# Performance work log

Measured on AMD Instinct MI355X. Metric: run time of the kernel, lower is better.

Reference implementation:

```python
import jax, jax.numpy as jnp
import numpy as np

B, Q, K, DQ, DK, DV, H = 4, 256, 1024, 512, 512, 512, 128
MASK_VALUE = -1e6  # matches torch sequence_mask fill of -1000000.0


def setup_inputs() -> dict:
    key = jax.random.key(0)
    ks = jax.random.split(key, 7)
    q = jax.random.normal(ks[0], (B, Q, DQ), dtype=jnp.float32)
    k = jax.random.normal(ks[1], (B, K, DK), dtype=jnp.float32)
    v = jax.random.normal(ks[2], (B, K, DV), dtype=jnp.float32)
    valid_lens = jax.random.randint(ks[3], (B,), 1, K + 1).astype(jnp.int64)
    # Linear weights stored torch-style as [out, in]
    w_q = jax.random.normal(ks[4], (H, DQ), dtype=jnp.float32) * 0.05
    w_k = jax.random.normal(ks[5], (H, DK), dtype=jnp.float32) * 0.05
    w_v = jax.random.normal(ks[6], (H,), dtype=jnp.float32) * 0.05
    return {"q": q, "k": k, "v": v, "valid_lens": valid_lens,
            "w_q": w_q, "w_k": w_k, "w_v": w_v}


def reference(q, k, v, valid_lens, w_q, w_k, w_v):
    qh = jnp.einsum("bqd,hd->bqh", q, w_q)              # [B,Q,H]
    kh = jnp.einsum("bkd,hd->bkh", k, w_k)              # [B,K,H]
    feats = jnp.tanh(qh[:, :, None, :] + kh[:, None, :, :])  # [B,Q,K,H]
    scores = jnp.einsum("bqkh,h->bqk", feats, w_v)      # [B,Q,K]
    mask = jnp.arange(K)[None, None, :] < valid_lens[:, None, None]
    scores = jnp.where(mask, scores, MASK_VALUE)
    attn = jax.nn.softmax(scores, axis=-1)              # dropout is identity (p=0)
    return jnp.einsum("bqk,bkv->bqv", attn, v)          # [B,Q,DV]
```

## Files before the change

### kernel.cpp

```cpp
#include <hip/hip_runtime.h>

#define B_ 4
#define Q_ 256
#define K_ 1024
#define D_ 512
#define H_ 128
#define DV_ 512
#define LOG2E 1.4426950408889634f


__global__ __launch_bounds__(256) void proj_part(
    const float* __restrict__ qin, const float* __restrict__ kin,
    const float* __restrict__ wq,  const float* __restrict__ wk,
    const int* __restrict__ valid_lens, float* __restrict__ psum)
{
    __shared__ float Xs[64][68];
    __shared__ float Ws[64][132];

    const int t = threadIdx.x, bid = blockIdx.x;
    const int ds = bid & 7, tile = bid >> 3;
    const int d0 = ds * 64;
    const float* X; const float* W;
    if (tile < 16) { X = qin + (size_t)tile * 64 * D_; W = wq; }
    else {
        int kt = tile - 16, b = kt >> 4, kr = (kt & 15) * 64;
        if (kr >= valid_lens[b]) return;
        X = kin + ((size_t)b * K_ + kr) * D_;
        W = wk;
    }
    const int R0 = tile * 64;

#pragma unroll
    for (int i = 0; i < 4; ++i) {
        int idx = t + i * 256;
        int row = idx >> 4, dq = (idx & 15) * 4;
        float4 xv = *(const float4*)&X[(size_t)row * D_ + d0 + dq];
        Xs[dq+0][row] = xv.x; Xs[dq+1][row] = xv.y;
        Xs[dq+2][row] = xv.z; Xs[dq+3][row] = xv.w;
    }
#pragma unroll
    for (int i = 0; i < 8; ++i) {
        int idx = t + i * 256;
        int h = idx >> 4, dq = (idx & 15) * 4;
        float4 wv = *(const float4*)&W[(size_t)h * D_ + d0 + dq];
        Ws[dq+0][h] = wv.x; Ws[dq+1][h] = wv.y;
        Ws[dq+2][h] = wv.z; Ws[dq+3][h] = wv.w;
    }
    __syncthreads();

    const int wid = t >> 6, lane = t & 63;
    const int r0 = (wid >> 1) * 32 + (lane >> 3) * 4;
    const int h0 = (wid & 1)  * 64 + (lane & 7)  * 8;
    float c[4][8] = {};

#pragma unroll 4
    for (int kk = 0; kk < 64; ++kk) {
        float xr[4], wr[8];
        *(float4*)&xr[0] = *(const float4*)&Xs[kk][r0];
        *(float4*)&wr[0] = *(const float4*)&Ws[kk][h0];
        *(float4*)&wr[4] = *(const float4*)&Ws[kk][h0 + 4];
#pragma unroll
        for (int i = 0; i < 4; ++i)
#pragma unroll
            for (int j = 0; j < 8; ++j) c[i][j] += xr[i] * wr[j];
    }

    float* outp = psum + ((size_t)ds * 5120 + R0) * 128;
#pragma unroll
    for (int i = 0; i < 4; ++i) {
        *(float4*)&outp[(size_t)(r0 + i) * 128 + h0]     = *(const float4*)&c[i][0];
        *(float4*)&outp[(size_t)(r0 + i) * 128 + h0 + 4] = *(const float4*)&c[i][4];
    }
}

__global__ __launch_bounds__(256) void proj_reduce(
    const float* __restrict__ psum, const int* __restrict__ valid_lens,
    float* __restrict__ qh_s, float4* __restrict__ kh4)
{
    int gid = blockIdx.x * 256 + threadIdx.x;
    int row = gid >> 5, c4 = gid & 31;
    int b = 0, kk = 0;
    if (row >= 1024) {
        int r = row - 1024;
        b = r >> 10; kk = r & 1023;
        if (kk >= valid_lens[b]) return;
    }
    float4 s = make_float4(0.f, 0.f, 0.f, 0.f);
#pragma unroll
    for (int ds = 0; ds < 8; ++ds) {
        float4 v = *(const float4*)&psum[((size_t)ds * 5120 + row) * 128 + c4 * 4];
        s.x += v.x; s.y += v.y; s.z += v.z; s.w += v.w;
    }
    const float SC = 2.0f * LOG2E;
    s.x *= SC; s.y *= SC; s.z *= SC; s.w *= SC;
    if (row < 1024) *(float4*)&qh_s[(size_t)row * 128 + c4 * 4] = s;
    else            kh4[((size_t)(b * 32 + c4)) * K_ + kk] = s;
}

__global__ __launch_bounds__(256) void attn_part(
    const float* __restrict__ qh_s, const float4* __restrict__ kh4,
    const float* __restrict__ wvg,  const int* __restrict__ valid_lens,
    const float* __restrict__ vin,
    float* __restrict__ s_part, float4* __restrict__ o_part)
{
    __shared__ float  qv[1024];
    __shared__ float  wvs[128];
    __shared__ float  ptmp[3][8][64];
    __shared__ float  p[8][64];
    __shared__ float4 otmp[8][128];

    const int t   = threadIdx.x;
    const int bid = blockIdx.x;
    const int qt  = bid & 31, kc = (bid >> 5) & 15, b = bid >> 9;
    const int q0  = qt * 8;
    const int vl  = valid_lens[b];
    const int kbase = kc * 64;
    if (kbase >= vl) return;
    const int klen = min(64, vl - kbase);

#pragma unroll
    for (int i = 0; i < 4; ++i)
        qv[t + i * 256] = qh_s[(size_t)(b*Q_ + q0) * H_ + t + i * 256];
    if (t < 128) wvs[t] = wvg[t] * (-2.0f * LOG2E);
    __syncthreads();

    const int k  = t & 63;
    const int hh = t >> 6;
    const bool active = k < klen;

    float acc[8] = {};
    if (active) {
        const float4* khp = kh4 + (size_t)b * 32 * K_ + (kbase + k)
                          + (size_t)(hh * 8) * K_;
        const int hq0 = hh * 8;
        float4 kxn = khp[0];
#pragma unroll
        for (int i = 0; i < 8; ++i) {
            float4 kx = kxn;
            int ni = (i < 7) ? i + 1 : 7;
            kxn = khp[(size_t)ni * K_];
            const int hq = hq0 + i;
            float w4[4], kxa[4];
            *(float4*)&w4[0]  = *(const float4*)&wvs[hq*4];
            *(float4*)&kxa[0] = kx;
#pragma unroll
            for (int qi = 0; qi < 8; ++qi) {
                float q4[4];
                *(float4*)&q4[0] = *(const float4*)&qv[qi*128 + hq*4];
#pragma unroll
                for (int j = 0; j < 4; ++j) {
                    float tt = __builtin_amdgcn_exp2f(q4[j] + kxa[j]);
                    float rr = __builtin_amdgcn_rcpf(tt + 1.0f);
                    acc[qi] = fmaf(w4[j], rr, acc[qi]);
                }
            }
        }
    }
    if (hh != 0) {
#pragma unroll
        for (int qi = 0; qi < 8; ++qi) ptmp[hh-1][qi][k] = acc[qi];
    }
    __syncthreads();

    if (hh == 0) {
        float psum8[8];
#pragma unroll
        for (int qi = 0; qi < 8; ++qi) {
            float a = acc[qi] + ptmp[0][qi][k] + ptmp[1][qi][k] + ptmp[2][qi][k];
            float e = active ? __builtin_amdgcn_exp2f(a) : 0.f;
            p[qi][k] = e;
            psum8[qi] = e;
        }
#pragma unroll
        for (int off = 32; off > 0; off >>= 1)
#pragma unroll
            for (int qi = 0; qi < 8; ++qi) psum8[qi] += __shfl_xor(psum8[qi], off);
        if (t == 0) {
#pragma unroll
            for (int qi = 0; qi < 8; ++qi)
                s_part[(size_t)(b*Q_ + q0 + qi) * 16 + kc] = psum8[qi];
        }
    }
    __syncthreads();

    const int col  = t & 127;
    const int half = t >> 7;
    const int kb2  = half * 32;
    const int ke2  = min(klen, kb2 + 32);
    const float4* vb = (const float4*)vin + (size_t)b * K_ * 128
                     + (size_t)kbase * 128;

    float4 o[8];
#pragma unroll
    for (int qi = 0; qi < 8; ++qi) o[qi] = make_float4(0.f, 0.f, 0.f, 0.f);

    int kk = kb2;
    const int nfull = (ke2 > kb2) ? ((ke2 - kb2) >> 2) : 0;
    if (nfull > 0) {
        float4 n0v = vb[(size_t)(kk+0)*128 + col];
        float4 n1v = vb[(size_t)(kk+1)*128 + col];
        float4 n2v = vb[(size_t)(kk+2)*128 + col];
        float4 n3v = vb[(size_t)(kk+3)*128 + col];
        for (int g = 0; g < nfull; ++g) {
            float4 v0 = n0v, v1 = n1v, v2 = n2v, v3 = n3v;
            int kn = kk + 4;
            if (g + 1 < nfull) {
                n0v = vb[(size_t)(kn+0)*128 + col];
                n1v = vb[(size_t)(kn+1)*128 + col];
                n2v = vb[(size_t)(kn+2)*128 + col];
                n3v = vb[(size_t)(kn+3)*128 + col];
            }
#pragma unroll
            for (int qi = 0; qi < 8; ++qi) {
                float4 pq = *(const float4*)&p[qi][kk];
                o[qi].x += pq.x*v0.x + pq.y*v1.x + pq.z*v2.x + pq.w*v3.x;
                o[qi].y += pq.x*v0.y + pq.y*v1.y + pq.z*v2.y + pq.w*v3.y;
                o[qi].z += pq.x*v0.z + pq.y*v1.z + pq.z*v2.z + pq.w*v3.z;
                o[qi].w += pq.x*v0.w + pq.y*v1.w + pq.z*v2.w + pq.w*v3.w;
            }
            kk = kn;
        }
    }
    for (; kk < ke2; ++kk) {
        float4 v0 = vb[(size_t)kk*128 + col];
#pragma unroll
        for (int qi = 0; qi < 8; ++qi) {
            float pk = p[qi][kk];
            o[qi].x += pk*v0.x; o[qi].y += pk*v0.y;
            o[qi].z += pk*v0.z; o[qi].w += pk*v0.w;
        }
    }

    if (half == 1) {
#pragma unroll
        for (int qi = 0; qi < 8; ++qi) otmp[qi][col] = o[qi];
    }
    __syncthreads();
    if (half == 0) {
#pragma unroll
        for (int qi = 0; qi < 8; ++qi) {
            float4 r = otmp[qi][col];
            o[qi].x += r.x; o[qi].y += r.y; o[qi].z += r.z; o[qi].w += r.w;
            o_part[((size_t)kc * 1024 + (b*Q_ + q0 + qi)) * 128 + col] = o[qi];
        }
    }
}

__global__ __launch_bounds__(256) void finalize_kernel(
    const float4* __restrict__ o_part, const float* __restrict__ s_part,
    const int* __restrict__ valid_lens, float4* __restrict__ out)
{
    int gid = blockIdx.x * 256 + threadIdx.x;
    int row = gid >> 7, col = gid & 127;
    int b = row >> 8;
    int nch = (valid_lens[b] + 63) >> 6;
    float ssum = 0.f;
    float4 o = make_float4(0.f, 0.f, 0.f, 0.f);
    for (int ch = 0; ch < nch; ++ch) {
        ssum += s_part[(size_t)row * 16 + ch];
        float4 r = o_part[((size_t)ch * 1024 + row) * 128 + col];
        o.x += r.x; o.y += r.y; o.z += r.z; o.w += r.w;
    }
    float rs = __builtin_amdgcn_rcpf(ssum);
    out[gid] = make_float4(o.x*rs, o.y*rs, o.z*rs, o.w*rs);
}

extern "C" void kernel_launch(void* const* d_in, const int* in_sizes, int n_in,
                              void* d_out, int out_size, void* d_ws, size_t ws_size,
                              hipStream_t stream)
{
    const float* q  = (const float*)d_in[0];
    const float* k  = (const float*)d_in[1];
    const float* v  = (const float*)d_in[2];
    const int*   vl = (const int*)d_in[3];
    const float* wq = (const float*)d_in[4];
    const float* wk = (const float*)d_in[5];
    const float* wv = (const float*)d_in[6];
    float* out = (float*)d_out;

    float* qh_s  = (float*)d_ws;
    float* kh4   = qh_s  + (size_t)B_*Q_*H_;
    float* s_prt = kh4   + (size_t)B_*H_*K_;
    float* o_prt = s_prt + (size_t)B_*Q_*16;
    float* psum  = o_prt + (size_t)16*B_*Q_*DV_;

    proj_part      <<<dim3(640),  dim3(256), 0, stream>>>(q, k, wq, wk, vl, psum);
    proj_reduce    <<<dim3(640),  dim3(256), 0, stream>>>(psum, vl, qh_s, (float4*)kh4);
    attn_part      <<<dim3(2048), dim3(256), 0, stream>>>(qh_s, (const float4*)kh4, wv, vl, v, s_prt, (float4*)o_prt);
    finalize_kernel<<<dim3(512),  dim3(256), 0, stream>>>((const float4*)o_prt, s_prt, vl, (float4*)out);
}
```

Baseline: 115.3 us.

## Fuse projection reduction via atomics and widen attention key chunks to 128

Removes the proj_reduce kernel and its partial-sum buffer. proj_part now pre-scales the weights and atomically accumulates its split-D partials straight into zeroed qh/kh buffers, with a memset added up front. Separately, attn_part now takes 128-key chunks with two head-halves per thread group instead of 64 keys with four, which halves the block count and the number of finalize partials. The trade-off is many scattered float atomics in a strided kh layout, an extra memset, and possibly lower occupancy from the doubled per-thread head loop.

Measured after the change: 295.6 us. 156% more time.

```diff
diff --git a/kernel.cpp b/kernel.cpp
--- a/kernel.cpp
+++ b/kernel.cpp
@@ -12,7 +12,8 @@
 __global__ __launch_bounds__(256) void proj_part(
     const float* __restrict__ qin, const float* __restrict__ kin,
     const float* __restrict__ wq,  const float* __restrict__ wk,
-    const int* __restrict__ valid_lens, float* __restrict__ psum)
+    const int* __restrict__ valid_lens,
+    float* __restrict__ qh_s, float* __restrict__ khf)
 {
     __shared__ float Xs[64][68];
     __shared__ float Ws[64][132];
@@ -21,14 +22,18 @@
     const int ds = bid & 7, tile = bid >> 3;
     const int d0 = ds * 64;
     const float* X; const float* W;
-    if (tile < 16) { X = qin + (size_t)tile * 64 * D_; W = wq; }
+    int kb = 0, kr0 = 0;
+    bool is_q;
+    if (tile < 16) { X = qin + (size_t)tile * 64 * D_; W = wq; is_q = true; }
     else {
-        int kt = tile - 16, b = kt >> 4, kr = (kt & 15) * 64;
-        if (kr >= valid_lens[b]) return;
-        X = kin + ((size_t)b * K_ + kr) * D_;
+        int kt = tile - 16; kb = kt >> 4; kr0 = (kt & 15) * 64;
+        if (kr0 >= valid_lens[kb]) return;
+        X = kin + ((size_t)kb * K_ + kr0) * D_;
         W = wk;
+        is_q = false;
     }
     const int R0 = tile * 64;
+    const float SC = 2.0f * LOG2E;
 
 #pragma unroll
     for (int i = 0; i < 4; ++i) {
@@ -43,8 +48,8 @@
         int idx = t + i * 256;
         int h = idx >> 4, dq = (idx & 15) * 4;
         float4 wv = *(const float4*)&W[(size_t)h * D_ + d0 + dq];
-        Ws[dq+0][h] = wv.x; Ws[dq+1][h] = wv.y;
-        Ws[dq+2][h] = wv.z; Ws[dq+3][h] = wv.w;
+        Ws[dq+0][h] = wv.x * SC; Ws[dq+1][h] = wv.y * SC;
+        Ws[dq+2][h] = wv.z * SC; Ws[dq+3][h] = wv.w * SC;
     }
     __syncthreads();
 
@@ -65,36 +70,25 @@
             for (int j = 0; j < 8; ++j) c[i][j] += xr[i] * wr[j];
     }
 
-    float* outp = psum + ((size_t)ds * 5120 + R0) * 128;
-#pragma unroll
-    for (int i = 0; i < 4; ++i) {
-        *(float4*)&outp[(size_t)(r0 + i) * 128 + h0]     = *(const float4*)&c[i][0];
-        *(float4*)&outp[(size_t)(r0 + i) * 128 + h0 + 4] = *(const float4*)&c[i][4];
-    }
-}
-
-__global__ __launch_bounds__(256) void proj_reduce(
-    const float* __restrict__ psum, const int* __restrict__ valid_lens,
-    float* __restrict__ qh_s, float4* __restrict__ kh4)
-{
-    int gid = blockIdx.x * 256 + threadIdx.x;
-    int row = gid >> 5, c4 = gid & 31;
-    int b = 0, kk = 0;
-    if (row >= 1024) {
-        int r = row - 1024;
-        b = r >> 10; kk = r & 1023;
-        if (kk >= valid_lens[b]) return;
-    }
-    float4 s = make_float4(0.f, 0.f, 0.f, 0.f);
-#pragma unroll
-    for (int ds = 0; ds < 8; ++ds) {
-        float4 v = *(const float4*)&psum[((size_t)ds * 5120 + row) * 128 + c4 * 4];
-        s.x += v.x; s.y += v.y; s.z += v.z; s.w += v.w;
-    }
-    const float SC = 2.0f * LOG2E;
-    s.x *= SC; s.y *= SC; s.z *= SC; s.w *= SC;
-    if (row < 1024) *(float4*)&qh_s[(size_t)row * 128 + c4 * 4] = s;
-    else            kh4[((size_t)(b * 32 + c4)) * K_ + kk] = s;
+    if (is_q) {
+#pragma unroll
+        for (int i = 0; i < 4; ++i) {
+            float* rp = qh_s + (size_t)(R0 + r0 + i) * 128 + h0;
+#pragma unroll
+            for (int j = 0; j < 8; ++j) atomicAdd(&rp[j], c[i][j]);
+        }
+    } else {
+#pragma unroll
+        for (int i = 0; i < 4; ++i) {
+            int kk = kr0 + r0 + i;
+#pragma unroll
+            for (int j = 0; j < 8; ++j) {
+                int h = h0 + j;
+                size_t idx = (((size_t)kb * 32 + (h >> 2)) * K_ + kk) * 4 + (h & 3);
+                atomicAdd(&khf[idx], c[i][j]);
+            }
+        }
+    }
 }
 
 __global__ __launch_bounds__(256) void attn_part(
@@ -105,18 +99,19 @@
 {
     __shared__ float  qv[1024];
     __shared__ float  wvs[128];
-    __shared__ float  ptmp[3][8][64];
-    __shared__ float  p[8][64];
+    __shared__ float  ptmp[8][128];
+    __shared__ float  p[8][128];
+    __shared__ float  sred[2][8];
     __shared__ float4 otmp[8][128];
 
     const int t   = threadIdx.x;
     const int bid = blockIdx.x;
-    const int qt  = bid & 31, kc = (bid >> 5) & 15, b = bid >> 9;
+    const int qt  = bid & 31, kc = (bid >> 5) & 7, b = bid >> 8;
     const int q0  = qt * 8;
     const int vl  = valid_lens[b];
-    const int kbase = kc * 64;
+    const int kbase = kc * 128;
     if (kbase >= vl) return;
-    const int klen = min(64, vl - kbase);
+    const int klen = min(128, vl - kbase);
 
 #pragma unroll
     for (int i = 0; i < 4; ++i)
@@ -124,22 +119,21 @@
     if (t < 128) wvs[t] = wvg[t] * (-2.0f * LOG2E);
     __syncthreads();
 
-    const int k  = t & 63;
-    const int hh = t >> 6;
+    const int k  = t & 127;
+    const int hh = t >> 7;
     const bool active = k < klen;
 
     float acc[8] = {};
     if (active) {
         const float4* khp = kh4 + (size_t)b * 32 * K_ + (kbase + k)
-                          + (size_t)(hh * 8) * K_;
-        const int hq0 = hh * 8;
+                          + (size_t)(hh * 16) * K_;
         float4 kxn = khp[0];
-#pragma unroll
-        for (int i = 0; i < 8; ++i) {
+#pragma unroll 4
+        for (int i = 0; i < 16; ++i) {
             float4 kx = kxn;
-            int ni = (i < 7) ? i + 1 : 7;
+            int ni = (i < 15) ? i + 1 : 15;
             kxn = khp[(size_t)ni * K_];
-            const int hq = hq0 + i;
+            const int hq = hh * 16 + i;
             float w4[4], kxa[4];
             *(float4*)&w4[0]  = *(const float4*)&wvs[hq*4];
             *(float4*)&kxa[0] = kx;
@@ -156,9 +150,9 @@
             }
         }
     }
-    if (hh != 0) {
-#pragma unroll
-        for (int qi = 0; qi < 8; ++qi) ptmp[hh-1][qi][k] = acc[qi];
+    if (hh == 1) {
+#pragma unroll
+        for (int qi = 0; qi < 8; ++qi) ptmp[qi][k] = acc[qi];
     }
     __syncthreads();
 
@@ -166,7 +160,7 @@
         float psum8[8];
 #pragma unroll
         for (int qi = 0; qi < 8; ++qi) {
-            float a = acc[qi] + ptmp[0][qi][k] + ptmp[1][qi][k] + ptmp[2][qi][k];
+            float a = acc[qi] + ptmp[qi][k];
             float e = active ? __builtin_amdgcn_exp2f(a) : 0.f;
             p[qi][k] = e;
             psum8[qi] = e;
@@ -175,18 +169,23 @@
         for (int off = 32; off > 0; off >>= 1)
 #pragma unroll
             for (int qi = 0; qi < 8; ++qi) psum8[qi] += __shfl_xor(psum8[qi], off);
-        if (t == 0) {
-#pragma unroll
-            for (int qi = 0; qi < 8; ++qi)
-                s_part[(size_t)(b*Q_ + q0 + qi) * 16 + kc] = psum8[qi];
-        }
-    }
-    __syncthreads();
+        if ((t & 63) == 0) {
+#pragma unroll
+            for (int qi = 0; qi < 8; ++qi) sred[t >> 6][qi] = psum8[qi];
+        }
+    }
+    __syncthreads();
+
+    if (t == 0) {
+#pragma unroll
+        for (int qi = 0; qi < 8; ++qi)
+            s_part[(size_t)(b*Q_ + q0 + qi) * 8 + kc] = sred[0][qi] + sred[1][qi];
+    }
 
     const int col  = t & 127;
     const int half = t >> 7;
-    const int kb2  = half * 32;
-    const int ke2  = min(klen, kb2 + 32);
+    const int kb2  = half * 64;
+    const int ke2  = min(klen, kb2 + 64);
     const float4* vb = (const float4*)vin + (size_t)b * K_ * 128
                      + (size_t)kbase * 128;
 
@@ -253,11 +252,11 @@
     int gid = blockIdx.x * 256 + threadIdx.x;
     int row = gid >> 7, col = gid & 127;
     int b = row >> 8;
-    int nch = (valid_lens[b] + 63) >> 6;
+    int nch = (valid_lens[b] + 127) >> 7;
     float ssum = 0.f;
     float4 o = make_float4(0.f, 0.f, 0.f, 0.f);
     for (int ch = 0; ch < nch; ++ch) {
-        ssum += s_part[(size_t)row * 16 + ch];
+        ssum += s_part[(size_t)row * 8 + ch];
         float4 r = o_part[((size_t)ch * 1024 + row) * 128 + col];
         o.x += r.x; o.y += r.y; o.z += r.z; o.w += r.w;
     }
@@ -281,11 +280,11 @@
     float* qh_s  = (float*)d_ws;
     float* kh4   = qh_s  + (size_t)B_*Q_*H_;
     float* s_prt = kh4   + (size_t)B_*H_*K_;
-    float* o_prt = s_prt + (size_t)B_*Q_*16;
-    float* psum  = o_prt + (size_t)16*B_*Q_*DV_;
-
-    proj_part      <<<dim3(640),  dim3(256), 0, stream>>>(q, k, wq, wk, vl, psum);
-    proj_reduce    <<<dim3(640),  dim3(256), 0, stream>>>(psum, vl, qh_s, (float4*)kh4);
-    attn_part      <<<dim3(2048), dim3(256), 0, stream>>>(qh_s, (const float4*)kh4, wv, vl, v, s_prt, (float4*)o_prt);
+    float* o_prt = s_prt + (size_t)B_*Q_*8;
+
+    hipMemsetAsync(qh_s, 0, (size_t)(B_*Q_*H_ + B_*H_*K_) * sizeof(float), stream);
+
+    proj_part      <<<dim3(640),  dim3(256), 0, stream>>>(q, k, wq, wk, vl, qh_s, kh4);
+    attn_part      <<<dim3(1024), dim3(256), 0, stream>>>(qh_s, (const float4*)kh4, wv, vl, v, s_prt, (float4*)o_prt);
     finalize_kernel<<<dim3(512),  dim3(256), 0, stream>>>((const float4*)o_prt, s_prt, vl, (float4*)out);
 }
```

## Retile projection GEMM with register-prefetched double chunks and swizzled LDS

Applied to the files above, without the earlier changes.

The projection kernel now uses 32-row tiles with four D-splits, each block covering two 64-wide chunks. The next chunk is prefetched into registers while the current one is computed, and LDS uses an XOR swizzle instead of padding to avoid bank conflicts. The reduce kernel sums four partials instead of eight, which cuts partial-sum traffic. In the attention kernel, the exp and row-sum work is spread across all four wavefronts rather than one, at the cost of an extra shared buffer and a small final write step.

New measurement: 115.3 us. No clear change (-0.0%).

```diff
diff --git a/kernel.cpp b/kernel.cpp
--- a/kernel.cpp
+++ b/kernel.cpp
@@ -14,63 +14,86 @@
     const float* __restrict__ wq,  const float* __restrict__ wk,
     const int* __restrict__ valid_lens, float* __restrict__ psum)
 {
-    __shared__ float Xs[64][68];
-    __shared__ float Ws[64][132];
+    __shared__ float Xs[64 * 32];
+    __shared__ float Ws[64 * 128];
 
     const int t = threadIdx.x, bid = blockIdx.x;
-    const int ds = bid & 7, tile = bid >> 3;
-    const int d0 = ds * 64;
+    const int ds = bid & 3, tile = bid >> 2;
     const float* X; const float* W;
-    if (tile < 16) { X = qin + (size_t)tile * 64 * D_; W = wq; }
+    int R0;
+    if (tile < 32) { X = qin + (size_t)tile * 32 * D_; W = wq; R0 = tile * 32; }
     else {
-        int kt = tile - 16, b = kt >> 4, kr = (kt & 15) * 64;
-        if (kr >= valid_lens[b]) return;
-        X = kin + ((size_t)b * K_ + kr) * D_;
+        int kt = tile - 32, kb = kt >> 5, kr0 = (kt & 31) * 32;
+        if (kr0 >= valid_lens[kb]) return;
+        X = kin + ((size_t)kb * K_ + kr0) * D_;
         W = wk;
-    }
-    const int R0 = tile * 64;
-
-#pragma unroll
-    for (int i = 0; i < 4; ++i) {
-        int idx = t + i * 256;
-        int row = idx >> 4, dq = (idx & 15) * 4;
-        float4 xv = *(const float4*)&X[(size_t)row * D_ + d0 + dq];
-        Xs[dq+0][row] = xv.x; Xs[dq+1][row] = xv.y;
-        Xs[dq+2][row] = xv.z; Xs[dq+3][row] = xv.w;
-    }
-#pragma unroll
-    for (int i = 0; i < 8; ++i) {
-        int idx = t + i * 256;
-        int h = idx >> 4, dq = (idx & 15) * 4;
-        float4 wv = *(const float4*)&W[(size_t)h * D_ + d0 + dq];
-        Ws[dq+0][h] = wv.x; Ws[dq+1][h] = wv.y;
-        Ws[dq+2][h] = wv.z; Ws[dq+3][h] = wv.w;
-    }
-    __syncthreads();
+        R0 = 1024 + kt * 32;
+    }
+
+    const int xrow  = (t + 0) >> 4, xdq = (t & 15) * 4;
+    const int xrow1 = (t + 256) >> 4;
+    float4 xr0, xr1, wr8[8];
+
+    #define LOADX(c) do { \
+        xr0 = *(const float4*)&X[(size_t)xrow  * D_ + (c)*64 + xdq]; \
+        xr1 = *(const float4*)&X[(size_t)xrow1 * D_ + (c)*64 + xdq]; } while (0)
+    #define LOADW(c) do { \
+        _Pragma("unroll") \
+        for (int i = 0; i < 8; ++i) { \
+            int idx = t + i * 256; \
+            wr8[i] = *(const float4*)&W[(size_t)(idx >> 4) * D_ + (c)*64 + (idx & 15) * 4]; } } while (0)
+    #define WRITE_LDS() do { \
+        { float v[4]; *(float4*)v = xr0; \
+          _Pragma("unroll") \
+          for (int j = 0; j < 4; ++j) { int d = xdq + j; \
+              Xs[d * 32 + (xrow ^ (((d >> 2) & 7) << 2))] = v[j]; } } \
+        { float v[4]; *(float4*)v = xr1; \
+          _Pragma("unroll") \
+          for (int j = 0; j < 4; ++j) { int d = xdq + j; \
+              Xs[d * 32 + (xrow1 ^ (((d >> 2) & 7) << 2))] = v[j]; } } \
+        _Pragma("unroll") \
+        for (int i = 0; i < 8; ++i) { \
+            int idx = t + i * 256; int h = idx >> 4, dq = (idx & 15) * 4; \
+            float v[4]; *(float4*)v = wr8[i]; \
+            _Pragma("unroll") \
+            for (int j = 0; j < 4; ++j) { int d = dq + j; \
+                Ws[d * 128 + (h ^ (((d >> 2) & 7) << 2))] = v[j]; } } } while (0)
 
     const int wid = t >> 6, lane = t & 63;
-    const int r0 = (wid >> 1) * 32 + (lane >> 3) * 4;
-    const int h0 = (wid & 1)  * 64 + (lane & 7)  * 8;
-    float c[4][8] = {};
-
-#pragma unroll 4
-    for (int kk = 0; kk < 64; ++kk) {
-        float xr[4], wr[8];
-        *(float4*)&xr[0] = *(const float4*)&Xs[kk][r0];
-        *(float4*)&wr[0] = *(const float4*)&Ws[kk][h0];
-        *(float4*)&wr[4] = *(const float4*)&Ws[kk][h0 + 4];
-#pragma unroll
-        for (int i = 0; i < 4; ++i)
-#pragma unroll
-            for (int j = 0; j < 8; ++j) c[i][j] += xr[i] * wr[j];
+    const int r0 = (lane & 7) * 4;
+    const int h0 = wid * 32 + (lane >> 3) * 4;
+    float c[4][4] = {};
+
+    const int c0 = ds * 2;
+    LOADX(c0); LOADW(c0);
+    WRITE_LDS();
+
+    for (int cc = 0; cc < 2; ++cc) {
+        __syncthreads();
+        if (cc < 1) { LOADX(c0 + 1); LOADW(c0 + 1); }
+#pragma unroll 8
+        for (int kk = 0; kk < 64; ++kk) {
+            const int xc = ((kk >> 2) & 7) << 2;
+            float xr[4], wr[4];
+            *(float4*)&xr[0] = *(const float4*)&Xs[kk * 32  + (r0 ^ xc)];
+            *(float4*)&wr[0] = *(const float4*)&Ws[kk * 128 + (h0 ^ xc)];
+#pragma unroll
+            for (int i = 0; i < 4; ++i)
+#pragma unroll
+                for (int j = 0; j < 4; ++j) c[i][j] = fmaf(xr[i], wr[j], c[i][j]);
+        }
+        __syncthreads();
+        if (cc < 1) WRITE_LDS();
     }
 
     float* outp = psum + ((size_t)ds * 5120 + R0) * 128;
 #pragma unroll
-    for (int i = 0; i < 4; ++i) {
-        *(float4*)&outp[(size_t)(r0 + i) * 128 + h0]     = *(const float4*)&c[i][0];
-        *(float4*)&outp[(size_t)(r0 + i) * 128 + h0 + 4] = *(const float4*)&c[i][4];
-    }
+    for (int i = 0; i < 4; ++i)
+        *(float4*)&outp[(size_t)(r0 + i) * 128 + h0] = *(const float4*)&c[i][0];
+
+    #undef LOADX
+    #undef LOADW
+    #undef WRITE_LDS
 }
 
 __global__ __launch_bounds__(256) void proj_reduce(
@@ -87,7 +110,7 @@
     }
     float4 s = make_float4(0.f, 0.f, 0.f, 0.f);
 #pragma unroll
-    for (int ds = 0; ds < 8; ++ds) {
+    for (int ds = 0; ds < 4; ++ds) {
         float4 v = *(const float4*)&psum[((size_t)ds * 5120 + row) * 128 + c4 * 4];
         s.x += v.x; s.y += v.y; s.z += v.z; s.w += v.w;
     }
@@ -105,8 +128,9 @@
 {
     __shared__ float  qv[1024];
     __shared__ float  wvs[128];
-    __shared__ float  ptmp[3][8][64];
+    __shared__ float  ptmp[4][8][64];
     __shared__ float  p[8][64];
+    __shared__ float  sred[8];
     __shared__ float4 otmp[8][128];
 
     const int t   = threadIdx.x;
@@ -156,32 +180,29 @@
             }
         }
     }
-    if (hh != 0) {
-#pragma unroll
-        for (int qi = 0; qi < 8; ++qi) ptmp[hh-1][qi][k] = acc[qi];
-    }
+#pragma unroll
+    for (int qi = 0; qi < 8; ++qi) ptmp[hh][qi][k] = acc[qi];
     __syncthreads();
 
-    if (hh == 0) {
-        float psum8[8];
-#pragma unroll
-        for (int qi = 0; qi < 8; ++qi) {
-            float a = acc[qi] + ptmp[0][qi][k] + ptmp[1][qi][k] + ptmp[2][qi][k];
+    {
+        const int qia = hh * 2;
+#pragma unroll
+        for (int q2 = 0; q2 < 2; ++q2) {
+            const int qi = qia + q2;
+            float a = ptmp[0][qi][k] + ptmp[1][qi][k]
+                    + ptmp[2][qi][k] + ptmp[3][qi][k];
             float e = active ? __builtin_amdgcn_exp2f(a) : 0.f;
             p[qi][k] = e;
-            psum8[qi] = e;
-        }
-#pragma unroll
-        for (int off = 32; off > 0; off >>= 1)
-#pragma unroll
-            for (int qi = 0; qi < 8; ++qi) psum8[qi] += __shfl_xor(psum8[qi], off);
-        if (t == 0) {
-#pragma unroll
-            for (int qi = 0; qi < 8; ++qi)
-                s_part[(size_t)(b*Q_ + q0 + qi) * 16 + kc] = psum8[qi];
+            float s = e;
+#pragma unroll
+            for (int off = 32; off > 0; off >>= 1) s += __shfl_xor(s, off);
+            if (k == 0) sred[qi] = s;
         }
     }
     __syncthreads();
+
+    if (t < 8)
+        s_part[(size_t)(b*Q_ + q0 + t) * 16 + kc] = sred[t];
 
     const int col  = t & 127;
     const int half = t >> 7;
```
